# Performance work log

Hardware: AMD Instinct MI355X
Metric: run time of the kernel (lower is better)

Reference implementation:

```python
import jax, jax.numpy as jnp
import numpy as np

IMG = 256
C = 8
B = 64
CENTER = (IMG - 1) / 2.0


def _grids():
    # gridy varies along rows, gridx along cols (torch.meshgrid default 'ij')
    g = jnp.arange(IMG, dtype=jnp.float32)
    gy, gx = jnp.meshgrid(g, g, indexing='ij')
    dists = jnp.sqrt((gx - CENTER) ** 2 + (gy - CENTER) ** 2)  # [H, W]
    pts = jnp.stack([gy, gx], axis=-1)  # [H, W, 2] with (y, x) order as in torch.cat([gridy, gridx], 1)
    return dists, pts


def setup_inputs() -> dict:
    key = jax.random.key(0)
    k1, k2 = jax.random.split(key)
    batch = jax.random.normal(k1, (B, C, IMG, IMG), dtype=jnp.float32)
    # odd-ish window diameters in [64, 256]; sizes[0] > 0 so the resize branch is taken
    sizes = jax.random.randint(k2, (B,), 64, IMG + 1, dtype=jnp.int32)
    return {"batch": batch, "sizes": sizes}


def reference(batch, sizes):
    dists, pts_grid = _grids()
    # radius per sample: (sizes - 1) / 2, mask where dist < radius + 0.5
    radius = (sizes.astype(jnp.float32) - 1.0) / 2.0 + 0.5  # [B]
    mask = dists[None, :, :] < radius[:, None, None]         # [B, H, W] bool

    # single-pass compaction of all three tensors with the same mask (eager, dynamic N)
    tex = jnp.transpose(batch, (0, 2, 3, 1))[mask]                              # [N, C]
    pts = jnp.broadcast_to(pts_grid[None], (batch.shape[0], IMG, IMG, 2))[mask]  # [N, 2]
    imgid = jnp.broadcast_to(
        jnp.arange(batch.shape[0], dtype=jnp.int32)[:, None, None],
        (batch.shape[0], IMG, IMG))[mask]                                        # [N]
    batch_size = jnp.array(batch.shape[0], dtype=jnp.int32)
    return tex, pts, imgid, batch_size
```

## Files before the change

### kernel.cpp

```cpp
#include <hip/hip_runtime.h>

#define IMG 256
#define NB 64
#define NCH 8
#define NROWS (NB * IMG)
#define PLANE (IMG * IMG)

__device__ __forceinline__ int isqrt_i(int x) {
    int t = (int)__builtin_sqrtf((float)x);
    t -= (t * t > x);
    t += ((t + 1) * (t + 1) <= x);
    return t;
}

__device__ __forceinline__ int row_count(int s, int h) {
    int ky = 2 * h - 255;
    int rem = s * s - ky * ky;
    if (rem < 2) return 0;
    int t = isqrt_i(rem - 1);
    int kx_max = (t & 1) ? t : t - 1;
    return kx_max + 1;
}

__global__ void setup_kernel(const int* __restrict__ sizes,
                             int* __restrict__ image_base,
                             float* __restrict__ out, int out_size) {
    __shared__ int acc[NB];
    __shared__ int s_sz[NB];
    int t = threadIdx.x;
    if (t < NB) { acc[t] = 0; s_sz[t] = sizes[t]; }
    __syncthreads();
    int b = t >> 4;
    int s = s_sz[b];
    int h0 = (t & 15) * 16;
    int sum = 0;
    #pragma unroll
    for (int k = 0; k < 16; ++k) sum += row_count(s, h0 + k);
    atomicAdd(&acc[b], sum);
    __syncthreads();
    if (t < NB) {
        int a = acc[t];
        int v = a;
        for (int d = 1; d < 64; d <<= 1) {
            int u = __shfl_up(v, d);
            if (t >= d) v += u;
        }
        image_base[t] = v - a;
    }
    if (t == 0) out[out_size - 1] = (float)NB;
}

__global__ void scatter_rows(const float* __restrict__ batch,
                             const int* __restrict__ sizes,
                             const int* __restrict__ image_base,
                             float* __restrict__ out, int N) {
    int row = blockIdx.x;
    int b = row >> 8;
    int h = row & 255;
    int t = threadIdx.x;
    int s = sizes[b];
    int cnt = row_count(s, h);
    if (cnt == 0) return;

    int c = (t < h) ? row_count(s, t) : 0;
    for (int o = 32; o; o >>= 1) c += __shfl_down(c, o);
    __shared__ int wsum[4];
    __shared__ int s_n0;
    if ((t & 63) == 0) wsum[t >> 6] = c;
    __syncthreads();
    if (t == 0) s_n0 = image_base[b] + wsum[0] + wsum[1] + wsum[2] + wsum[3];
    __syncthreads();

    int lo = (255 - (cnt - 1)) >> 1;
    if (t < lo || t >= lo + cnt) return;
    int n = s_n0 + (t - lo);

    const float* bp = batch + (size_t)b * NCH * PLANE + h * IMG + t;
    float4 t0, t1;
    t0.x = bp[0 * PLANE]; t0.y = bp[1 * PLANE];
    t0.z = bp[2 * PLANE]; t0.w = bp[3 * PLANE];
    t1.x = bp[4 * PLANE]; t1.y = bp[5 * PLANE];
    t1.z = bp[6 * PLANE]; t1.w = bp[7 * PLANE];

    float4* texp = (float4*)(out + (size_t)n * 8);
    texp[0] = t0;
    texp[1] = t1;

    float2* ptsp = (float2*)(out + (size_t)N * 8 + (size_t)n * 2);
    *ptsp = make_float2((float)h, (float)t);

    out[(size_t)N * 10 + n] = (float)b;
}

extern "C" void kernel_launch(void* const* d_in, const int* in_sizes, int n_in,
                              void* d_out, int out_size, void* d_ws, size_t ws_size,
                              hipStream_t stream) {
    const float* batch = (const float*)d_in[0];
    const int* sizes = (const int*)d_in[1];
    float* out = (float*)d_out;

    int N = (out_size - 1) / 11;

    int* image_base = (int*)d_ws;

    setup_kernel<<<1, 1024, 0, stream>>>(sizes, image_base, out, out_size);
    scatter_rows<<<NROWS, 256, 0, stream>>>(batch, sizes, image_base, out, N);
}
```

Baseline: 30.17 us.

## Stage row loads through LDS with vectorized per-channel reads in scatter kernel

The scatter kernel now has each 32-thread group load one channel's row segment as float4 vectors and transpose it through a padded shared-memory tile. This replaces eight strided scalar loads per pixel. The global loads are issued before the prefix-count reduction so they overlap with it. The setup kernel also replaces shared atomics with a shuffle reduction. The cost is an extra barrier, about 9 KB of LDS per block, and LDS transpose traffic.

```diff
diff --git a/kernel.cpp b/kernel.cpp
--- a/kernel.cpp
+++ b/kernel.cpp
@@ -5,6 +5,9 @@
 #define NCH 8
 #define NROWS (NB * IMG)
 #define PLANE (IMG * IMG)
+
+typedef float vf4 __attribute__((ext_vector_type(4)));
+typedef float vf2 __attribute__((ext_vector_type(2)));
 
 __device__ __forceinline__ int isqrt_i(int x) {
     int t = (int)__builtin_sqrtf((float)x);
@@ -25,35 +28,36 @@
 __global__ void setup_kernel(const int* __restrict__ sizes,
                              int* __restrict__ image_base,
                              float* __restrict__ out, int out_size) {
-    __shared__ int acc[NB];
-    __shared__ int s_sz[NB];
+    __shared__ int tot[NB];
     int t = threadIdx.x;
-    if (t < NB) { acc[t] = 0; s_sz[t] = sizes[t]; }
-    __syncthreads();
     int b = t >> 4;
-    int s = s_sz[b];
     int h0 = (t & 15) * 16;
+    int s = sizes[b];
     int sum = 0;
     #pragma unroll
     for (int k = 0; k < 16; ++k) sum += row_count(s, h0 + k);
-    atomicAdd(&acc[b], sum);
+    #pragma unroll
+    for (int d = 1; d < 16; d <<= 1) sum += __shfl_down(sum, d);
+    if ((t & 15) == 0) tot[b] = sum;
     __syncthreads();
     if (t < NB) {
-        int a = acc[t];
-        int v = a;
-        for (int d = 1; d < 64; d <<= 1) {
-            int u = __shfl_up(v, d);
-            if (t >= d) v += u;
+        int a = tot[t];
+        int iv = a;
+        #pragma unroll
+        for (int d = 1; d < NB; d <<= 1) {
+            int u = __shfl_up(iv, d);
+            if (t >= d) iv += u;
         }
-        image_base[t] = v - a;
+        image_base[t] = iv - a;
     }
     if (t == 0) out[out_size - 1] = (float)NB;
 }
 
-__global__ void scatter_rows(const float* __restrict__ batch,
-                             const int* __restrict__ sizes,
-                             const int* __restrict__ image_base,
-                             float* __restrict__ out, int N) {
+__global__ void __launch_bounds__(256) scatter_rows(
+        const float* __restrict__ batch,
+        const int* __restrict__ sizes,
+        const int* __restrict__ image_base,
+        float* __restrict__ out, int N) {
     int row = blockIdx.x;
     int b = row >> 8;
     int h = row & 255;
@@ -61,33 +65,54 @@
     int s = sizes[b];
     int cnt = row_count(s, h);
     if (cnt == 0) return;
+    int lo = (255 - (cnt - 1)) >> 1;
+    int hi = lo + cnt;
+    int lo4 = lo & ~3;
 
-    int c = (t < h) ? row_count(s, t) : 0;
-    for (int o = 32; o; o >>= 1) c += __shfl_down(c, o);
+    int c = t >> 5;
+    int l32 = t & 31;
+    const float* cp = batch + (size_t)b * NCH * PLANE + (size_t)c * PLANE + h * IMG;
+    int px0 = lo4 + l32 * 4;
+    int px1 = lo4 + (32 + l32) * 4;
+    bool pa = px0 < hi, pb = px1 < hi;
+    vf4 va, vb;
+    if (pa) va = *(const vf4*)(cp + px0);
+    if (pb) vb = *(const vf4*)(cp + px1);
+
+    int cc = (t < h) ? row_count(s, t) : 0;
+    #pragma unroll
+    for (int o = 32; o; o >>= 1) cc += __shfl_down(cc, o);
     __shared__ int wsum[4];
     __shared__ int s_n0;
-    if ((t & 63) == 0) wsum[t >> 6] = c;
+    if ((t & 63) == 0) wsum[t >> 6] = cc;
+
+    __shared__ float lds[IMG * 9];
+    if (pa) {
+        #pragma unroll
+        for (int k = 0; k < 4; ++k) lds[(px0 + k) * 9 + c] = va[k];
+    }
+    if (pb) {
+        #pragma unroll
+        for (int k = 0; k < 4; ++k) lds[(px1 + k) * 9 + c] = vb[k];
+    }
     __syncthreads();
     if (t == 0) s_n0 = image_base[b] + wsum[0] + wsum[1] + wsum[2] + wsum[3];
     __syncthreads();
 
-    int lo = (255 - (cnt - 1)) >> 1;
-    if (t < lo || t >= lo + cnt) return;
-    int n = s_n0 + (t - lo);
+    int w = t;
+    if (w < lo || w >= hi) return;
+    int n = s_n0 + (w - lo);
 
-    const float* bp = batch + (size_t)b * NCH * PLANE + h * IMG + t;
-    float4 t0, t1;
-    t0.x = bp[0 * PLANE]; t0.y = bp[1 * PLANE];
-    t0.z = bp[2 * PLANE]; t0.w = bp[3 * PLANE];
-    t1.x = bp[4 * PLANE]; t1.y = bp[5 * PLANE];
-    t1.z = bp[6 * PLANE]; t1.w = bp[7 * PLANE];
+    vf4 t0, t1;
+    t0.x = lds[w * 9 + 0]; t0.y = lds[w * 9 + 1];
+    t0.z = lds[w * 9 + 2]; t0.w = lds[w * 9 + 3];
+    t1.x = lds[w * 9 + 4]; t1.y = lds[w * 9 + 5];
+    t1.z = lds[w * 9 + 6]; t1.w = lds[w * 9 + 7];
+    *(vf4*)(out + (size_t)n * 8) = t0;
+    *(vf4*)(out + (size_t)n * 8 + 4) = t1;
 
-    float4* texp = (float4*)(out + (size_t)n * 8);
-    texp[0] = t0;
-    texp[1] = t1;
-
-    float2* ptsp = (float2*)(out + (size_t)N * 8 + (size_t)n * 2);
-    *ptsp = make_float2((float)h, (float)t);
+    vf2 p; p.x = (float)h; p.y = (float)w;
+    *(vf2*)(out + (size_t)N * 8 + (size_t)n * 2) = p;
 
     out[(size_t)N * 10 + n] = (float)b;
 }
```

Result: no change. 30.00 us (-0.6%).
